# Kernel optimization log

Measured on AMD Instinct MI355X. Metric: run time of the kernel, lower is better.

Reference implementation:

```python
import jax, jax.numpy as jnp
import numpy as np

N_NODES = 100000
N_EDGES = 1600000
HIDDEN = 128
NUM_LAYERS = 3
NUM_CLASSES = 16
NUM_GRAPHS = 64


def gcn_conv(x, src, dst, W, b):
    # x: [N, C_in] -> [N, C_out]; symmetric-normalized aggregation (self-loops
    # already appended to src/dst by the caller).
    n = x.shape[0]
    h = x @ W  # [N, C]
    deg = jax.ops.segment_sum(jnp.ones_like(dst, dtype=h.dtype), dst, num_segments=n)
    dinv = jnp.where(deg > 0, jax.lax.rsqrt(deg), 0.0)  # D^{-1/2}
    norm = dinv[src] * dinv[dst]  # [E+N]
    msg = h[src] * norm[:, None]  # gather + scale
    out = jax.ops.segment_sum(msg, dst, num_segments=n)  # scatter-add
    return out + b


def setup_inputs() -> dict:
    key = jax.random.key(0)
    k = jax.random.split(key, 8)
    x = jax.random.normal(k[0], (N_NODES, HIDDEN), dtype=jnp.float32)
    edge_index = jax.random.randint(k[1], (2, N_EDGES), 0, N_NODES, dtype=jnp.int64)
    batch = jnp.sort(jax.random.randint(k[2], (N_NODES,), 0, NUM_GRAPHS, dtype=jnp.int64))
    scale = 1.0 / np.sqrt(HIDDEN)
    Ws = jax.random.uniform(k[3], (NUM_LAYERS, HIDDEN, HIDDEN), jnp.float32, -scale, scale)
    bs = jax.random.uniform(k[4], (NUM_LAYERS, HIDDEN), jnp.float32, -scale, scale)
    lin_W = jax.random.uniform(k[5], (HIDDEN, NUM_CLASSES), jnp.float32, -scale, scale)
    lin_b = jax.random.uniform(k[6], (NUM_CLASSES,), jnp.float32, -scale, scale)
    return {"x": x, "edge_index": edge_index, "batch": batch,
            "Ws": Ws, "bs": bs, "lin_W": lin_W, "lin_b": lin_b}


def reference(x, edge_index, batch, Ws, bs, lin_W, lin_b):
    n = x.shape[0]
    loops = jnp.arange(n, dtype=edge_index.dtype)
    src = jnp.concatenate([edge_index[0], loops])
    dst = jnp.concatenate([edge_index[1], loops])
    for l in range(NUM_LAYERS - 1):
        x = jax.nn.relu(gcn_conv(x, src, dst, Ws[l], bs[l]))
    x = gcn_conv(x, src, dst, Ws[-1], bs[-1])
    # global mean pool over graphs
    sums = jax.ops.segment_sum(x, batch, num_segments=NUM_GRAPHS)
    cnts = jax.ops.segment_sum(jnp.ones((n,), x.dtype), batch, num_segments=NUM_GRAPHS)
    pooled = sums / jnp.maximum(cnts, 1.0)[:, None]
    # dropout p=0.5 is identity in eval mode
    return pooled @ lin_W + lin_b
```

## Files before the change

kernel.cpp:

```cpp
#include <hip/hip_runtime.h>
#include <math.h>

#define N_NODES    100000
#define N_EDGES    1600000
#define HIDDEN     128
#define NUM_GRAPHS 64

constexpr int POOL_CHUNKS = 16;

constexpr int BINSHIFT = 10;
constexpr int BINSZ    = 1 << BINSHIFT;
constexpr int NBIN     = (N_NODES + BINSZ - 1) / BINSZ;
constexpr int CH_E     = 8192;
constexpr int NCH      = (N_EDGES + CH_E - 1) / CH_E;
constexpr int CAP1     = 160;
constexpr int CAP2     = 18432;


static __device__ __forceinline__ unsigned short f2bf(float f) {
    unsigned u = __float_as_uint(f);
    u += 0x7FFFu + ((u >> 16) & 1u);
    return (unsigned short)(u >> 16);
}
static __device__ __forceinline__ float b2f(unsigned short h) {
    return __uint_as_float(((unsigned)h) << 16);
}


typedef float floatx2 __attribute__((ext_vector_type(2)));
typedef short bf16x8  __attribute__((ext_vector_type(8)));
typedef float f32x4v  __attribute__((ext_vector_type(4)));

#if __has_builtin(__builtin_amdgcn_cvt_pk_f32_fp8) && __has_builtin(__builtin_amdgcn_cvt_pk_fp8_f32)
#define FP8_HW 1
#else
#define FP8_HW 0
#endif

static __device__ __forceinline__ float4 dec4_e4m3(unsigned u) {
#if FP8_HW
    floatx2 lo = __builtin_amdgcn_cvt_pk_f32_fp8((int)u, false);
    floatx2 hi = __builtin_amdgcn_cvt_pk_f32_fp8((int)u, true);
    return make_float4(lo[0], lo[1], hi[0], hi[1]);
#else
    float t[4];
    #pragma unroll
    for (int i = 0; i < 4; ++i) {
        unsigned x = (u >> (8 * i)) & 0xFFu;
        unsigned s = x >> 7, e = (x >> 3) & 15u, m = x & 7u;
        float fn = __uint_as_float((s << 31) | ((e + 120u) << 23) | (m << 20));
        float fs = (float)m * 0.001953125f;
        if (s) fs = -fs;
        t[i] = e ? fn : fs;
    }
    return make_float4(t[0], t[1], t[2], t[3]);
#endif
}

static __device__ __forceinline__ unsigned char enc1_e4m3(float v) {
    unsigned u = __float_as_uint(v);
    unsigned s = u >> 31;
    float a = fabsf(v);
    if (a >= 448.f) return (unsigned char)((s << 7) | 0x7Eu);
    if (a < 0.015625f) {
        unsigned q = (unsigned)rintf(a * 512.f);
        return (unsigned char)((s << 7) | q);
    }
    unsigned au = u & 0x7FFFFFFFu;
    au += 0x7FFFFu + ((au >> 20) & 1u);
    unsigned e = (au >> 23) - 120u;
    unsigned m = (au >> 20) & 7u;
    if (e >= 15u && m >= 7u) { e = 15u; m = 6u; }
    return (unsigned char)((s << 7) | (e << 3) | m);
}

static __device__ __forceinline__ unsigned enc4_e4m3(float a, float b, float c, float d) {
#if FP8_HW
    int v = 0;
    v = __builtin_amdgcn_cvt_pk_fp8_f32(a, b, v, false);
    v = __builtin_amdgcn_cvt_pk_fp8_f32(c, d, v, true);
    return (unsigned)v;
#else
    return (unsigned)enc1_e4m3(a) | ((unsigned)enc1_e4m3(b) << 8) |
           ((unsigned)enc1_e4m3(c) << 16) | ((unsigned)enc1_e4m3(d) << 24);
#endif
}


__global__ void k_gbounds(const int* __restrict__ batch, int* __restrict__ gstart) {
    int i = blockIdx.x * blockDim.x + threadIdx.x;
    if (i >= N_NODES) return;
    int b = batch[i];
    if (i == 0) {
        for (int g = 0; g <= b; ++g) gstart[g] = 0;
    } else {
        int bp = batch[i - 1];
        for (int g = bp + 1; g <= b; ++g) gstart[g] = i;
    }
    if (i == N_NODES - 1) {
        for (int g = b + 1; g <= NUM_GRAPHS; ++g) gstart[g] = N_NODES;
    }
}


__global__ __launch_bounds__(256) void k_p1(const int* __restrict__ src,
                                            const int* __restrict__ dst,
                                            unsigned* __restrict__ slab,
                                            int* __restrict__ gcnt) {
    __shared__ unsigned bl[NBIN * CAP1];
    __shared__ int c1[NBIN];

    const int ch = blockIdx.x;
    const int t  = threadIdx.x;
    for (int i = t; i < NBIN; i += 256) c1[i] = 0;
    __syncthreads();

    const int e0 = ch * CH_E;
    const int e1 = (e0 + CH_E < N_EDGES) ? e0 + CH_E : N_EDGES;
    for (int e = e0 + t; e < e1; e += 256) {
        int d = dst[e];
        int s = src[e];
        int b = d >> BINSHIFT;
        int pos = atomicAdd(&c1[b], 1);
        if (pos < CAP1)
            bl[b * CAP1 + pos] = ((unsigned)s << BINSHIFT) | (unsigned)(d & (BINSZ - 1));
    }
    __syncthreads();

    const int wv = t >> 6, ln = t & 63;
    for (int b = wv; b < NBIN; b += 4) {
        int n = c1[b]; n = n < CAP1 ? n : CAP1;
        unsigned* sp = &slab[((size_t)b * NCH + ch) * CAP1];
        for (int i = ln; i < n; i += 64) sp[i] = bl[b * CAP1 + i];
        if (ln == 0) gcnt[b * NCH + ch] = n;
    }
}


__global__ void k_binscan(const int* __restrict__ gcnt, int* __restrict__ binbase) {
    __shared__ int T[NBIN];
    int t = threadIdx.x;
    if (t < NBIN) {
        int s = 0;
        for (int c = 0; c < NCH; ++c) s += gcnt[t * NCH + c];
        T[t] = s;
    }
    __syncthreads();
    if (t == 0) {
        int run = 0;
        for (int b = 0; b < NBIN; ++b) { binbase[b] = run; run += T[b]; }
        binbase[NBIN] = run;
    }
}


__global__ __launch_bounds__(1024) void k_p2(const unsigned* __restrict__ slab,
                                             const int* __restrict__ gcnt,
                                             const int* __restrict__ binbase,
                                             int* __restrict__ csr_src,
                                             int* __restrict__ offs,
                                             float* __restrict__ dinv) {
    __shared__ unsigned eb[CAP2];
    __shared__ int cnt2[BINSZ];
    __shared__ int off2[BINSZ];
    __shared__ int cur[BINSZ];
    __shared__ int choff[NCH + 1];
    __shared__ int csc[256];

    const int bin = blockIdx.x;
    const int t   = threadIdx.x;

    cnt2[t] = 0; cur[t] = 0;
    if (t < 256) csc[t] = (t < NCH) ? gcnt[bin * NCH + t] : 0;
    __syncthreads();

    for (int off = 1; off < 256; off <<= 1) {
        int add = 0;
        if (t < 256 && t >= off) add = csc[t - off];
        __syncthreads();
        if (t < 256) csc[t] += add;
        __syncthreads();
    }
    if (t < NCH) {
        int v = gcnt[bin * NCH + t];
        choff[t] = csc[t] - v;
        if (t == NCH - 1) choff[NCH] = csc[t];
    }
    __syncthreads();
    int total = choff[NCH]; total = total < CAP2 ? total : CAP2;

    const int wv = t >> 6, ln = t & 63;
    for (int c = wv; c < NCH; c += 16) {
        int o = choff[c];
        int n = choff[c + 1] - o;
        const unsigned* sp = &slab[((size_t)bin * NCH + c) * CAP1];
        for (int i = ln; i < n; i += 64) {
            int idx = o + i;
            if (idx < CAP2) {
                unsigned v = sp[i];
                eb[idx] = v;
                atomicAdd(&cnt2[v & (BINSZ - 1)], 1);
            }
        }
    }
    __syncthreads();

    int mycnt = cnt2[t];
    off2[t] = mycnt;
    __syncthreads();
    for (int off = 1; off < BINSZ; off <<= 1) {
        int add = (t >= off) ? off2[t - off] : 0;
        __syncthreads();
        off2[t] += add;
        __syncthreads();
    }
    int excl = off2[t] - mycnt;
    __syncthreads();
    off2[t] = excl;
    __syncthreads();

    const int base  = binbase[bin];
    const int node0 = bin << BINSHIFT;
    int node = node0 + t;
    if (node < N_NODES) {
        offs[node] = base + excl;
        dinv[node] = rsqrtf((float)(mycnt + 1));
    }
    if (bin == NBIN - 1 && t == 0) offs[N_NODES] = base + total;
    __syncthreads();

    for (int i = t; i < total; i += 1024) {
        unsigned v = eb[i];
        int lo = v & (BINSZ - 1);
        int p = atomicAdd(&cur[lo], 1);
        csr_src[base + off2[lo] + p] = (int)(v >> BINSHIFT);
    }
}


__global__ __launch_bounds__(256) void k_wprep(const float* __restrict__ Ws,
                                               unsigned short* __restrict__ Wt_g) {
    int idx = blockIdx.x * 256 + threadIdx.x;
    if (idx >= 2 * HIDDEN * HIDDEN) return;
    int l = idx >> 14, rem = idx & 16383, c = rem >> 7, k = rem & 127;
    Wt_g[idx] = f2bf(Ws[l * HIDDEN * HIDDEN + k * HIDDEN + c]);
}


template <bool IN_F32>
__global__ __launch_bounds__(256) void k_gemm(const void* __restrict__ Xin,
                                              const unsigned short* __restrict__ Wt_g,
                                              const float* __restrict__ dinv,
                                              unsigned char* __restrict__ Hb8) {
    __shared__ char sm[70144];
    unsigned short* Xl = (unsigned short*)sm;
    unsigned short* Wl = (unsigned short*)(sm + 34816);
    float*          Dl = (float*)(sm + 69632);
    unsigned char*  Hl = (unsigned char*)sm;

    const int t    = threadIdx.x;
    const int row0 = blockIdx.x * 128;
    const float* Xf = (const float*)Xin;
    const unsigned short* Xb = (const unsigned short*)Xin;

    #pragma unroll
    for (int i = 0; i < 8; ++i) {
        int idx = t + i * 256;
        int r = idx >> 4, kq = idx & 15;
        int rg = row0 + r; rg = rg < N_NODES ? rg : N_NODES - 1;
        if (IN_F32) {
            float4 xa = *(const float4*)&Xf[(size_t)rg * HIDDEN + kq * 8];
            float4 xb = *(const float4*)&Xf[(size_t)rg * HIDDEN + kq * 8 + 4];
            unsigned short o[8];
            o[0] = f2bf(xa.x); o[1] = f2bf(xa.y); o[2] = f2bf(xa.z); o[3] = f2bf(xa.w);
            o[4] = f2bf(xb.x); o[5] = f2bf(xb.y); o[6] = f2bf(xb.z); o[7] = f2bf(xb.w);
            *(uint4*)&Xl[r * 136 + kq * 8] = *(uint4*)o;
        } else {
            *(uint4*)&Xl[r * 136 + kq * 8] = *(const uint4*)&Xb[(size_t)rg * HIDDEN + kq * 8];
        }
        *(uint4*)&Wl[r * 136 + kq * 8] = *(const uint4*)&Wt_g[r * HIDDEN + kq * 8];
    }
    if (t < 128) {
        int rg = row0 + t; rg = rg < N_NODES ? rg : N_NODES - 1;
        Dl[t] = dinv[rg] * 8.f;
    }
    __syncthreads();

    const int lane = t & 63;
    const int wv   = t >> 6;
    const int rb0  = wv * 32;
    const int arow = lane & 15;
    const int kgrp = lane >> 4;

    f32x4v c[2][8];
    #pragma unroll
    for (int rb = 0; rb < 2; ++rb)
        #pragma unroll
        for (int cb = 0; cb < 8; ++cb)
            c[rb][cb] = (f32x4v){0.f, 0.f, 0.f, 0.f};

    #pragma unroll
    for (int kc = 0; kc < 4; ++kc) {
        int kbase = kc * 32 + kgrp * 8;
        bf16x8 a0 = *(const bf16x8*)&Xl[(rb0 + arow) * 136 + kbase];
        bf16x8 a1 = *(const bf16x8*)&Xl[(rb0 + 16 + arow) * 136 + kbase];
        #pragma unroll
        for (int cb = 0; cb < 8; ++cb) {
            bf16x8 b = *(const bf16x8*)&Wl[(cb * 16 + arow) * 136 + kbase];
            c[0][cb] = __builtin_amdgcn_mfma_f32_16x16x32_bf16(a0, b, c[0][cb], 0, 0, 0);
            c[1][cb] = __builtin_amdgcn_mfma_f32_16x16x32_bf16(a1, b, c[1][cb], 0, 0, 0);
        }
    }
    __syncthreads();

    const int col   = lane & 15;
    const int rbase = (lane >> 4) * 4;
    #pragma unroll
    for (int rb = 0; rb < 2; ++rb) {
        #pragma unroll
        for (int cb = 0; cb < 8; ++cb) {
            int rl = rb0 + rb * 16 + rbase;
            f32x4v cv = c[rb][cb];
            unsigned p = enc4_e4m3(cv[0] * Dl[rl], cv[1] * Dl[rl + 1],
                                   cv[2] * Dl[rl + 2], cv[3] * Dl[rl + 3]);
            int cc = cb * 16 + col;
            Hl[(rl + 0) * 128 + cc] = (unsigned char)(p & 0xFF);
            Hl[(rl + 1) * 128 + cc] = (unsigned char)((p >> 8) & 0xFF);
            Hl[(rl + 2) * 128 + cc] = (unsigned char)((p >> 16) & 0xFF);
            Hl[(rl + 3) * 128 + cc] = (unsigned char)((p >> 24) & 0xFF);
        }
    }
    __syncthreads();

    #pragma unroll
    for (int i = 0; i < 4; ++i) {
        int q = t + i * 256;
        int r = q >> 3, qq = q & 7;
        int row = row0 + r;
        if (row < N_NODES)
            *(uint4*)&Hb8[(size_t)row * HIDDEN + qq * 16] = *(const uint4*)&Hl[r * 128 + qq * 16];
    }
}


template <int OUT_MODE, bool BIAS, bool RELU>
__global__ __launch_bounds__(256) void k_aggregate(const unsigned char* __restrict__ Hb8,
                                                   const int* __restrict__ offs,
                                                   const int* __restrict__ csr_src,
                                                   const float* __restrict__ dinv,
                                                   const float* __restrict__ bias,
                                                   void* __restrict__ outv,
                                                   float in_dec, float out_enc) {
    int g    = threadIdx.x >> 5;
    int lane = threadIdx.x & 31;
    int node = blockIdx.x * 8 + g;
    if (node >= N_NODES) return;
    int c4 = lane * 4;

    float di = dinv[node];
    float4 acc = dec4_e4m3(*(const unsigned*)&Hb8[(size_t)node * HIDDEN + c4]);

    int j0 = offs[node], j1 = offs[node + 1];
    #pragma unroll 4
    for (int j = j0; j < j1; ++j) {
        int s = csr_src[j];
        float4 v = dec4_e4m3(*(const unsigned*)&Hb8[(size_t)s * HIDDEN + c4]);
        acc.x += v.x; acc.y += v.y; acc.z += v.z; acc.w += v.w;
    }

    float ms = di * in_dec;
    acc.x *= ms; acc.y *= ms; acc.z *= ms; acc.w *= ms;
    if (BIAS) {
        float4 bv = *(const float4*)&bias[c4];
        acc.x += bv.x; acc.y += bv.y; acc.z += bv.z; acc.w += bv.w;
    }
    if (RELU) {
        acc.x = fmaxf(acc.x, 0.f); acc.y = fmaxf(acc.y, 0.f);
        acc.z = fmaxf(acc.z, 0.f); acc.w = fmaxf(acc.w, 0.f);
    }
    if (OUT_MODE == 1) {
        float es = di * out_enc;
        unsigned p = enc4_e4m3(acc.x * es, acc.y * es, acc.z * es, acc.w * es);
        *(unsigned*)&((unsigned char*)outv)[(size_t)node * HIDDEN + c4] = p;
    } else if (OUT_MODE == 2) {
        ushort4 o;
        o.x = f2bf(acc.x); o.y = f2bf(acc.y); o.z = f2bf(acc.z); o.w = f2bf(acc.w);
        *(ushort4*)&((unsigned short*)outv)[(size_t)node * HIDDEN + c4] = o;
    } else {
        *(float4*)&((float*)outv)[(size_t)node * HIDDEN + c4] = acc;
    }
}


__global__ __launch_bounds__(256) void k_pool2(const float* __restrict__ X,
                                               const int* __restrict__ gstart,
                                               float* __restrict__ part) {
    int g  = blockIdx.x;
    int ch = blockIdx.y;
    int start = gstart[g], end = gstart[g + 1];
    int len = end - start;
    int r0 = start + (int)((long long)len * ch / POOL_CHUNKS);
    int r1 = start + (int)((long long)len * (ch + 1) / POOL_CHUNKS);

    int rp = threadIdx.x >> 5;
    int c4 = (threadIdx.x & 31) * 4;

    float4 acc = make_float4(0.f, 0.f, 0.f, 0.f);
    for (int r = r0 + rp; r < r1; r += 8) {
        float4 v = *(const float4*)&X[(size_t)r * HIDDEN + c4];
        acc.x += v.x; acc.y += v.y; acc.z += v.z; acc.w += v.w;
    }

    __shared__ float4 sh[256];
    sh[threadIdx.x] = acc;
    __syncthreads();
    #pragma unroll
    for (int off = 4; off >= 1; off >>= 1) {
        if (rp < off) {
            float4 o = sh[(rp + off) * 32 + (threadIdx.x & 31)];
            float4 m = sh[threadIdx.x];
            m.x += o.x; m.y += o.y; m.z += o.z; m.w += o.w;
            sh[threadIdx.x] = m;
        }
        __syncthreads();
    }
    if (rp == 0) {
        float4 v = sh[threadIdx.x];
        *(float4*)&part[((size_t)g * POOL_CHUNKS + ch) * HIDDEN + c4] = v;
    }
}


__global__ void k_final(const float* __restrict__ part, const int* __restrict__ gstart,
                        const float* __restrict__ W2, const float* __restrict__ b2,
                        const float* __restrict__ linW, const float* __restrict__ linb,
                        float* __restrict__ out) {
    __shared__ float m[HIDDEN];
    __shared__ float t[HIDDEN];
    int g = blockIdx.x;
    int c = threadIdx.x;
    float s = 0.f;
    #pragma unroll
    for (int ch = 0; ch < POOL_CHUNKS; ++ch)
        s += part[((size_t)g * POOL_CHUNKS + ch) * HIDDEN + c];
    float cnt = fmaxf((float)(gstart[g + 1] - gstart[g]), 1.0f);
    m[c] = s / cnt;
    __syncthreads();
    float acc = b2[c];
    #pragma unroll 4
    for (int k = 0; k < HIDDEN; ++k) acc += m[k] * W2[k * HIDDEN + c];
    t[c] = acc;
    __syncthreads();
    if (c < 16) {
        float o = linb[c];
        #pragma unroll 4
        for (int k = 0; k < HIDDEN; ++k) o += t[k] * linW[k * 16 + c];
        out[g * 16 + c] = o;
    }
}


extern "C" void kernel_launch(void* const* d_in, const int* in_sizes, int n_in,
                              void* d_out, int out_size, void* d_ws, size_t ws_size,
                              hipStream_t stream) {
    const float* x     = (const float*)d_in[0];
    const int*   edge  = (const int*)d_in[1];
    const int*   batch = (const int*)d_in[2];
    const float* Ws    = (const float*)d_in[3];
    const float* bs    = (const float*)d_in[4];
    const float* linW  = (const float*)d_in[5];
    const float* linb  = (const float*)d_in[6];
    float* out = (float*)d_out;

    const int* src = edge;
    const int* dst = edge + N_EDGES;

    float* bufA = (float*)d_ws;
    unsigned* slab = (unsigned*)bufA;
    float* bufBreg = bufA + (size_t)N_NODES * HIDDEN;
    unsigned char* hb8  = (unsigned char*)bufBreg;
    unsigned char* x2b8 = (unsigned char*)bufBreg + (size_t)N_NODES * HIDDEN;
    unsigned short* x1b = (unsigned short*)((unsigned char*)bufBreg + (size_t)2 * N_NODES * HIDDEN);
    float* dinv = bufBreg + (size_t)N_NODES * HIDDEN;
    float* part = dinv + N_NODES;
    int* offs    = (int*)(part + NUM_GRAPHS * POOL_CHUNKS * HIDDEN);
    int* csr_src = offs + N_NODES + 1;
    int* gstart  = csr_src + N_EDGES;
    int* gcnt    = gstart + NUM_GRAPHS + 1;
    int* binbase = gcnt + NBIN * NCH;
    unsigned short* Wt_g = (unsigned short*)(binbase + NBIN + 1);

    const int NB_N    = (N_NODES + 255) / 256;
    const int NB_ROW  = N_NODES / 8;
    const int NB_GEMM = (N_NODES + 127) / 128;

    k_p1<<<NCH, 256, 0, stream>>>(src, dst, slab, gcnt);
    k_binscan<<<1, 128, 0, stream>>>(gcnt, binbase);
    k_p2<<<NBIN, 1024, 0, stream>>>(slab, gcnt, binbase, csr_src, offs, dinv);
    k_gbounds<<<NB_N, 256, 0, stream>>>(batch, gstart);
    k_wprep<<<(2 * HIDDEN * HIDDEN + 255) / 256, 256, 0, stream>>>(Ws, Wt_g);

    k_gemm<true><<<NB_GEMM, 256, 0, stream>>>(x, Wt_g, dinv, hb8);
    k_aggregate<2, true, true><<<NB_ROW, 256, 0, stream>>>(hb8, offs, csr_src, dinv, bs, x1b, 0.125f, 0.f);

    k_gemm<false><<<NB_GEMM, 256, 0, stream>>>(x1b, Wt_g + HIDDEN * HIDDEN, dinv, hb8);
    k_aggregate<1, true, true><<<NB_ROW, 256, 0, stream>>>(hb8, offs, csr_src, dinv, bs + HIDDEN, x2b8, 0.125f, 32.f);

    k_aggregate<0, false, false><<<NB_ROW, 256, 0, stream>>>(x2b8, offs, csr_src, dinv, nullptr, bufA, 0.03125f, 0.f);
    k_pool2<<<dim3(NUM_GRAPHS, POOL_CHUNKS), 256, 0, stream>>>(bufA, gstart, part);

    k_final<<<NUM_GRAPHS, HIDDEN, 0, stream>>>(part, gstart,
                                               Ws + 2 * HIDDEN * HIDDEN, bs + 2 * HIDDEN,
                                               linW, linb, out);
}
```

Measured before the change: 247.9 us.

## Widen aggregate gathers to 16B per lane and fuse last aggregation with pooling

The aggregate kernels now assign 8 lanes per node, each loading 16 fp8 channels with a uint4 gather, and use two independent accumulators to raise memory-level parallelism. The final-layer aggregation is fused with global mean pooling: per-block node sums are reduced in shared memory by graph id and atomically added into a per-graph buffer that is zeroed in the bin-scan kernel. This removes the full fp32 N×128 write and read of the last layer's output and the separate pool kernel, at the cost of float atomics and some non-deterministic summation order. The bounds checks on the node index were dropped, which relies on N_NODES being divisible by 32.

Result: faster. 224.2 us (-9.5%).

```diff
diff --git a/kernel.cpp b/kernel.cpp
--- a/kernel.cpp
+++ b/kernel.cpp
@@ -86,6 +86,14 @@
 #endif
 }
 
+static __device__ __forceinline__ void dec16(uint4 v, float* f) {
+    float4 a = dec4_e4m3(v.x), b = dec4_e4m3(v.y), c = dec4_e4m3(v.z), d = dec4_e4m3(v.w);
+    f[0]=a.x; f[1]=a.y; f[2]=a.z; f[3]=a.w;
+    f[4]=b.x; f[5]=b.y; f[6]=b.z; f[7]=b.w;
+    f[8]=c.x; f[9]=c.y; f[10]=c.z; f[11]=c.w;
+    f[12]=d.x; f[13]=d.y; f[14]=d.z; f[15]=d.w;
+}
+
 
 __global__ void k_gbounds(const int* __restrict__ batch, int* __restrict__ gstart) {
     int i = blockIdx.x * blockDim.x + threadIdx.x;
@@ -137,9 +145,11 @@
 }
 
 
-__global__ void k_binscan(const int* __restrict__ gcnt, int* __restrict__ binbase) {
+__global__ void k_binscan(const int* __restrict__ gcnt, int* __restrict__ binbase,
+                          float* __restrict__ part) {
     __shared__ int T[NBIN];
     int t = threadIdx.x;
+    for (int i = t; i < NUM_GRAPHS * HIDDEN; i += 128) part[i] = 0.f;
     if (t < NBIN) {
         int s = 0;
         for (int c = 0; c < NCH; ++c) s += gcnt[t * NCH + c];
@@ -351,82 +361,132 @@
                                                    const float* __restrict__ bias,
                                                    void* __restrict__ outv,
                                                    float in_dec, float out_enc) {
-    int g    = threadIdx.x >> 5;
-    int lane = threadIdx.x & 31;
-    int node = blockIdx.x * 8 + g;
-    if (node >= N_NODES) return;
-    int c4 = lane * 4;
+    int g    = threadIdx.x >> 3;
+    int lane = threadIdx.x & 7;
+    int node = blockIdx.x * 32 + g;
+    int c16  = lane * 16;
 
     float di = dinv[node];
-    float4 acc = dec4_e4m3(*(const unsigned*)&Hb8[(size_t)node * HIDDEN + c4]);
+    float accA[16], accB[16];
+    dec16(*(const uint4*)&Hb8[(size_t)node * HIDDEN + c16], accA);
+    #pragma unroll
+    for (int i = 0; i < 16; ++i) accB[i] = 0.f;
 
     int j0 = offs[node], j1 = offs[node + 1];
-    #pragma unroll 4
-    for (int j = j0; j < j1; ++j) {
-        int s = csr_src[j];
-        float4 v = dec4_e4m3(*(const unsigned*)&Hb8[(size_t)s * HIDDEN + c4]);
-        acc.x += v.x; acc.y += v.y; acc.z += v.z; acc.w += v.w;
+    int j = j0;
+    #pragma unroll 2
+    for (; j + 2 <= j1; j += 2) {
+        int s0 = csr_src[j], s1 = csr_src[j + 1];
+        uint4 v0 = *(const uint4*)&Hb8[(size_t)s0 * HIDDEN + c16];
+        uint4 v1 = *(const uint4*)&Hb8[(size_t)s1 * HIDDEN + c16];
+        float f0[16], f1[16];
+        dec16(v0, f0); dec16(v1, f1);
+        #pragma unroll
+        for (int i = 0; i < 16; ++i) { accA[i] += f0[i]; accB[i] += f1[i]; }
+    }
+    if (j < j1) {
+        uint4 v0 = *(const uint4*)&Hb8[(size_t)csr_src[j] * HIDDEN + c16];
+        float f0[16];
+        dec16(v0, f0);
+        #pragma unroll
+        for (int i = 0; i < 16; ++i) accA[i] += f0[i];
     }
 
     float ms = di * in_dec;
-    acc.x *= ms; acc.y *= ms; acc.z *= ms; acc.w *= ms;
+    float acc[16];
+    #pragma unroll
+    for (int i = 0; i < 16; ++i) acc[i] = (accA[i] + accB[i]) * ms;
     if (BIAS) {
-        float4 bv = *(const float4*)&bias[c4];
-        acc.x += bv.x; acc.y += bv.y; acc.z += bv.z; acc.w += bv.w;
+        #pragma unroll
+        for (int q = 0; q < 4; ++q) {
+            float4 bv = *(const float4*)&bias[c16 + q * 4];
+            acc[q * 4 + 0] += bv.x; acc[q * 4 + 1] += bv.y;
+            acc[q * 4 + 2] += bv.z; acc[q * 4 + 3] += bv.w;
+        }
     }
     if (RELU) {
-        acc.x = fmaxf(acc.x, 0.f); acc.y = fmaxf(acc.y, 0.f);
-        acc.z = fmaxf(acc.z, 0.f); acc.w = fmaxf(acc.w, 0.f);
+        #pragma unroll
+        for (int i = 0; i < 16; ++i) acc[i] = fmaxf(acc[i], 0.f);
     }
     if (OUT_MODE == 1) {
         float es = di * out_enc;
-        unsigned p = enc4_e4m3(acc.x * es, acc.y * es, acc.z * es, acc.w * es);
-        *(unsigned*)&((unsigned char*)outv)[(size_t)node * HIDDEN + c4] = p;
-    } else if (OUT_MODE == 2) {
-        ushort4 o;
-        o.x = f2bf(acc.x); o.y = f2bf(acc.y); o.z = f2bf(acc.z); o.w = f2bf(acc.w);
-        *(ushort4*)&((unsigned short*)outv)[(size_t)node * HIDDEN + c4] = o;
+        uint4 p;
+        p.x = enc4_e4m3(acc[0] * es,  acc[1] * es,  acc[2] * es,  acc[3] * es);
+        p.y = enc4_e4m3(acc[4] * es,  acc[5] * es,  acc[6] * es,  acc[7] * es);
+        p.z = enc4_e4m3(acc[8] * es,  acc[9] * es,  acc[10] * es, acc[11] * es);
+        p.w = enc4_e4m3(acc[12] * es, acc[13] * es, acc[14] * es, acc[15] * es);
+        *(uint4*)&((unsigned char*)outv)[(size_t)node * HIDDEN + c16] = p;
     } else {
-        *(float4*)&((float*)outv)[(size_t)node * HIDDEN + c4] = acc;
-    }
-}
-
-
-__global__ __launch_bounds__(256) void k_pool2(const float* __restrict__ X,
-                                               const int* __restrict__ gstart,
-                                               float* __restrict__ part) {
-    int g  = blockIdx.x;
-    int ch = blockIdx.y;
-    int start = gstart[g], end = gstart[g + 1];
-    int len = end - start;
-    int r0 = start + (int)((long long)len * ch / POOL_CHUNKS);
-    int r1 = start + (int)((long long)len * (ch + 1) / POOL_CHUNKS);
-
-    int rp = threadIdx.x >> 5;
-    int c4 = (threadIdx.x & 31) * 4;
-
-    float4 acc = make_float4(0.f, 0.f, 0.f, 0.f);
-    for (int r = r0 + rp; r < r1; r += 8) {
-        float4 v = *(const float4*)&X[(size_t)r * HIDDEN + c4];
-        acc.x += v.x; acc.y += v.y; acc.z += v.z; acc.w += v.w;
-    }
-
-    __shared__ float4 sh[256];
-    sh[threadIdx.x] = acc;
-    __syncthreads();
-    #pragma unroll
-    for (int off = 4; off >= 1; off >>= 1) {
-        if (rp < off) {
-            float4 o = sh[(rp + off) * 32 + (threadIdx.x & 31)];
-            float4 m = sh[threadIdx.x];
-            m.x += o.x; m.y += o.y; m.z += o.z; m.w += o.w;
-            sh[threadIdx.x] = m;
+        unsigned short o[16];
+        #pragma unroll
+        for (int i = 0; i < 16; ++i) o[i] = f2bf(acc[i]);
+        *(uint4*)&((unsigned short*)outv)[(size_t)node * HIDDEN + c16]     = *(uint4*)&o[0];
+        *(uint4*)&((unsigned short*)outv)[(size_t)node * HIDDEN + c16 + 8] = *(uint4*)&o[8];
+    }
+}
+
+
+__global__ __launch_bounds__(256) void k_aggpool(const unsigned char* __restrict__ Hb8,
+                                                 const int* __restrict__ offs,
+                                                 const int* __restrict__ csr_src,
+                                                 const float* __restrict__ dinv,
+                                                 const int* __restrict__ batch,
+                                                 float* __restrict__ part,
+                                                 float in_dec) {
+    __shared__ float lacc[32][128];
+    __shared__ int gid[32];
+
+    int g    = threadIdx.x >> 3;
+    int lane = threadIdx.x & 7;
+    int node = blockIdx.x * 32 + g;
+    int c16  = lane * 16;
+
+    float di = dinv[node];
+    float accA[16], accB[16];
+    dec16(*(const uint4*)&Hb8[(size_t)node * HIDDEN + c16], accA);
+    #pragma unroll
+    for (int i = 0; i < 16; ++i) accB[i] = 0.f;
+
+    int j0 = offs[node], j1 = offs[node + 1];
+    int j = j0;
+    #pragma unroll 2
+    for (; j + 2 <= j1; j += 2) {
+        int s0 = csr_src[j], s1 = csr_src[j + 1];
+        uint4 v0 = *(const uint4*)&Hb8[(size_t)s0 * HIDDEN + c16];
+        uint4 v1 = *(const uint4*)&Hb8[(size_t)s1 * HIDDEN + c16];
+        float f0[16], f1[16];
+        dec16(v0, f0); dec16(v1, f1);
+        #pragma unroll
+        for (int i = 0; i < 16; ++i) { accA[i] += f0[i]; accB[i] += f1[i]; }
+    }
+    if (j < j1) {
+        uint4 v0 = *(const uint4*)&Hb8[(size_t)csr_src[j] * HIDDEN + c16];
+        float f0[16];
+        dec16(v0, f0);
+        #pragma unroll
+        for (int i = 0; i < 16; ++i) accA[i] += f0[i];
+    }
+
+    float ms = di * in_dec;
+    #pragma unroll
+    for (int i = 0; i < 16; ++i) lacc[g][c16 + i] = (accA[i] + accB[i]) * ms;
+    if (lane == 0) gid[g] = batch[node];
+    __syncthreads();
+
+    if (threadIdx.x < 128) {
+        int c = threadIdx.x;
+        float run = 0.f;
+        int curg = gid[0];
+        #pragma unroll 4
+        for (int r = 0; r < 32; ++r) {
+            int gg = gid[r];
+            if (gg != curg) {
+                atomicAdd(&part[curg * HIDDEN + c], run);
+                run = 0.f; curg = gg;
+            }
+            run += lacc[r][c];
         }
-        __syncthreads();
-    }
-    if (rp == 0) {
-        float4 v = sh[threadIdx.x];
-        *(float4*)&part[((size_t)g * POOL_CHUNKS + ch) * HIDDEN + c4] = v;
+        atomicAdd(&part[curg * HIDDEN + c], run);
     }
 }
 
@@ -439,12 +499,8 @@
     __shared__ float t[HIDDEN];
     int g = blockIdx.x;
     int c = threadIdx.x;
-    float s = 0.f;
-    #pragma unroll
-    for (int ch = 0; ch < POOL_CHUNKS; ++ch)
-        s += part[((size_t)g * POOL_CHUNKS + ch) * HIDDEN + c];
     float cnt = fmaxf((float)(gstart[g + 1] - gstart[g]), 1.0f);
-    m[c] = s / cnt;
+    m[c] = part[g * HIDDEN + c] / cnt;
     __syncthreads();
     float acc = b2[c];
     #pragma unroll 4
@@ -491,23 +547,22 @@
     unsigned short* Wt_g = (unsigned short*)(binbase + NBIN + 1);
 
     const int NB_N    = (N_NODES + 255) / 256;
-    const int NB_ROW  = N_NODES / 8;
+    const int NB_AGG  = N_NODES / 32;
     const int NB_GEMM = (N_NODES + 127) / 128;
 
     k_p1<<<NCH, 256, 0, stream>>>(src, dst, slab, gcnt);
-    k_binscan<<<1, 128, 0, stream>>>(gcnt, binbase);
+    k_binscan<<<1, 128, 0, stream>>>(gcnt, binbase, part);
     k_p2<<<NBIN, 1024, 0, stream>>>(slab, gcnt, binbase, csr_src, offs, dinv);
     k_gbounds<<<NB_N, 256, 0, stream>>>(batch, gstart);
     k_wprep<<<(2 * HIDDEN * HIDDEN + 255) / 256, 256, 0, stream>>>(Ws, Wt_g);
 
     k_gemm<true><<<NB_GEMM, 256, 0, stream>>>(x, Wt_g, dinv, hb8);
-    k_aggregate<2, true, true><<<NB_ROW, 256, 0, stream>>>(hb8, offs, csr_src, dinv, bs, x1b, 0.125f, 0.f);
+    k_aggregate<2, true, true><<<NB_AGG, 256, 0, stream>>>(hb8, offs, csr_src, dinv, bs, x1b, 0.125f, 0.f);
 
     k_gemm<false><<<NB_GEMM, 256, 0, stream>>>(x1b, Wt_g + HIDDEN * HIDDEN, dinv, hb8);
-    k_aggregate<1, true, true><<<NB_ROW, 256, 0, stream>>>(hb8, offs, csr_src, dinv, bs + HIDDEN, x2b8, 0.125f, 32.f);
-
-    k_aggregate<0, false, false><<<NB_ROW, 256, 0, stream>>>(x2b8, offs, csr_src, dinv, nullptr, bufA, 0.03125f, 0.f);
-    k_pool2<<<dim3(NUM_GRAPHS, POOL_CHUNKS), 256, 0, stream>>>(bufA, gstart, part);
+    k_aggregate<1, true, true><<<NB_AGG, 256, 0, stream>>>(hb8, offs, csr_src, dinv, bs + HIDDEN, x2b8, 0.125f, 32.f);
+
+    k_aggpool<<<NB_AGG, 256, 0, stream>>>(x2b8, offs, csr_src, dinv, batch, part, 0.03125f);
 
     k_final<<<NUM_GRAPHS, HIDDEN, 0, stream>>>(part, gstart,
                                                Ws + 2 * HIDDEN * HIDDEN, bs + 2 * HIDDEN,
```
